# Optimization experiments

Measured on AMD Instinct MI355X. Metric: run time of the kernel, lower is better.

Reference implementation:

```python
import jax, jax.numpy as jnp
import numpy as np
import math

B, N, D, H, FF, L = 256, 200, 128, 8, 512, 2
KD = D // H  # key/val dim per head
NEG_INF = -1e30  # used via -jnp.inf where safe


def setup_inputs() -> dict:
    key = jax.random.key(0)
    ks = jax.random.split(key, 32)
    s = 0.08
    inp = {
        "coords": jax.random.uniform(ks[0], (B, N, 2), jnp.float32),
        "demand": jax.random.uniform(ks[1], (B, N), jnp.float32) * 0.01,
        # init embeddings
        "w_depot": jax.random.normal(ks[2], (2, D), jnp.float32) * s,
        "b_depot": jax.random.normal(ks[3], (D,), jnp.float32) * s,
        "w_init": jax.random.normal(ks[4], (3, D), jnp.float32) * s,
        "b_init": jax.random.normal(ks[5], (D,), jnp.float32) * s,
        # encoder layers (stacked over L)
        "Wq": jax.random.normal(ks[6], (L, H, D, KD), jnp.float32) * s,
        "Wk": jax.random.normal(ks[7], (L, H, D, KD), jnp.float32) * s,
        "Wv": jax.random.normal(ks[8], (L, H, D, KD), jnp.float32) * s,
        "Wo": jax.random.normal(ks[9], (L, H, KD, D), jnp.float32) * s,
        "ff1_w": jax.random.normal(ks[10], (L, D, FF), jnp.float32) * s,
        "ff1_b": jax.random.normal(ks[11], (L, FF), jnp.float32) * s,
        "ff2_w": jax.random.normal(ks[12], (L, FF, D), jnp.float32) * s,
        "ff2_b": jax.random.normal(ks[13], (L, D), jnp.float32) * s,
        "n1_g": jnp.ones((L, D), jnp.float32),
        "n1_b": jnp.zeros((L, D), jnp.float32),
        "n2_g": jnp.ones((L, D), jnp.float32),
        "n2_b": jnp.zeros((L, D), jnp.float32),
        # decoder projections
        "w_proj_nodes": jax.random.normal(ks[14], (D, 3 * D), jnp.float32) * s,
        "w_fixed": jax.random.normal(ks[15], (D, D), jnp.float32) * s,
        "w_step": jax.random.normal(ks[16], (D + 1, D), jnp.float32) * s,
        "w_out": jax.random.normal(ks[17], (D, D), jnp.float32) * s,
    }
    return inp


def _batch_norm(x, g, b):
    # torch BatchNorm1d on flattened (B*N, D), training-mode batch stats
    m = x.mean(axis=(0, 1))
    v = x.var(axis=(0, 1))
    return g * (x - m) * jax.lax.rsqrt(v + 1e-5) + b


def _mha(x, Wq, Wk, Wv, Wo):
    # x: [B,N,D]; W*: [H,D,KD]; Wo: [H,KD,D]
    Q = jnp.einsum('bni,hik->hbnk', x, Wq)
    K = jnp.einsum('bni,hik->hbnk', x, Wk)
    V = jnp.einsum('bni,hik->hbnk', x, Wv)
    scale = 1.0 / math.sqrt(KD)
    attn = jax.nn.softmax(scale * jnp.einsum('hbnk,hbmk->hbnm', Q, K), axis=-1)
    heads = jnp.einsum('hbnm,hbmk->hbnk', attn, V)
    return jnp.einsum('hbnk,hkd->bnd', heads, Wo)


def _forward(coords, demand, w_depot, b_depot, w_init, b_init,
             Wq, Wk, Wv, Wo, ff1_w, ff1_b, ff2_w, ff2_b,
             n1_g, n1_b, n2_g, n2_b, w_proj_nodes, w_fixed, w_step, w_out):
    # ---- _init_embed ----
    depot_emb = coords[:, :1, :2] @ w_depot + b_depot                      # [B,1,D]
    node_feat = jnp.concatenate([coords[:, 1:, :], demand[:, 1:, None]], -1)
    node_emb = node_feat @ w_init + b_init                                 # [B,N-1,D]
    h = jnp.concatenate([depot_emb, node_emb], axis=1)                     # [B,N,D]

    # ---- GraphAttentionEncoder ----
    for l in range(L):
        h = _batch_norm(h + _mha(h, Wq[l], Wk[l], Wv[l], Wo[l]), n1_g[l], n1_b[l])
        ff = jnp.maximum(h @ ff1_w[l] + ff1_b[l], 0.0) @ ff2_w[l] + ff2_b[l]
        h = _batch_norm(h + ff, n2_g[l], n2_b[l])

    # ---- _precompute ----
    fixed_ctx = h.mean(axis=1) @ w_fixed                                   # [B,D]
    proj = h @ w_proj_nodes                                                # [B,N,3D]
    gk, gv, lk = jnp.split(proj, 3, axis=-1)
    gk = gk.reshape(B, N, H, KD).transpose(2, 0, 1, 3)                     # [H,B,N,KD]
    gv = gv.reshape(B, N, H, KD).transpose(2, 0, 1, 3)                     # [H,B,N,KD]

    inv_sqrt_kd = 1.0 / math.sqrt(KD)
    inv_sqrt_d = 1.0 / math.sqrt(D)
    barange = jnp.arange(B)

    def step(carry, _):
        visited, cur, used = carry
        cur_emb = h[barange, cur]                                          # [B,D]
        ctx = jnp.concatenate([cur_emb, (1.0 - used)[:, None]], -1)        # [B,D+1]
        q = fixed_ctx + ctx @ w_step                                       # [B,D]
        qh = q.reshape(B, H, KD).transpose(1, 0, 2)                        # [H,B,KD]
        compat = jnp.einsum('hbk,hbnk->hbn', qh, gk) * inv_sqrt_kd         # [H,B,N]
        compat = jnp.where(visited[None], -jnp.inf, compat)                # mask_inner
        attn = jax.nn.softmax(compat, axis=-1)
        gl = jnp.einsum('hbn,hbnk->hbk', attn, gv)                         # [H,B,KD]
        final_q = gl.transpose(1, 0, 2).reshape(B, D) @ w_out              # [B,D]
        logits = jnp.einsum('bd,bnd->bn', final_q, lk) * inv_sqrt_d
        logits = jnp.tanh(logits) * 10.0                                   # tanh_clipping
        logits = jnp.where(visited, -jnp.inf, logits)                      # mask_logits
        logp = jax.nn.log_softmax(logits, axis=-1)                         # temp = 1.0
        sel = jnp.argmax(logp, axis=-1)                                    # greedy decode
        visited = visited.at[barange, sel].set(True)
        used = used + demand[barange, sel]
        return (visited, sel, used), (logp, sel)

    visited0 = jnp.zeros((B, N), bool).at[:, 0].set(True)  # start at depot
    cur0 = jnp.zeros((B,), jnp.int32)
    used0 = jnp.zeros((B,), jnp.float32)
    _, (logps, sels) = jax.lax.scan(step, (visited0, cur0, used0), None, length=N - 1)
    log_p = logps.transpose(1, 0, 2)   # [B, N-1, N]
    pi = sels.transpose(1, 0)          # [B, N-1]
    return log_p, pi


def reference(coords, demand, w_depot, b_depot, w_init, b_init,
              Wq, Wk, Wv, Wo, ff1_w, ff1_b, ff2_w, ff2_b,
              n1_g, n1_b, n2_g, n2_b, w_proj_nodes, w_fixed, w_step, w_out):
    return _forward(coords, demand, w_depot, b_depot, w_init, b_init,
                    Wq, Wk, Wv, Wo, ff1_w, ff1_b, ff2_w, ff2_b,
                    n1_g, n1_b, n2_g, n2_b, w_proj_nodes, w_fixed, w_step, w_out)
```

## Files before the change

kernel.cpp:

```cpp
#include <hip/hip_runtime.h>
#include <math.h>

#define NB 256
#define NN 200
#define ND 128
#define NH 8
#define NFF 512
#define MROWS (NB*NN)

#define NEG_BIG (-1.0e30f)

#define GBM 128
#define GBN 128
#define GBK 16
__global__ __launch_bounds__(256) void k_gemm(const float* __restrict__ A,
    const float* __restrict__ B, const float* __restrict__ bias,
    float* __restrict__ C, int M, int N, int K, int flags)
{
  __shared__ float As[GBK][GBM];
  __shared__ float Bs[GBK][GBN];
  const int t = threadIdx.x;
  const int tx = t & 15, ty = t >> 4;
  const int row0 = blockIdx.y * GBM, col0 = blockIdx.x * GBN;
  float acc[8][8] = {};
  for (int k0 = 0; k0 < K; k0 += GBK) {
    {
      int m = t >> 1, kb = (t & 1) * 8;
      const float* src = A + (size_t)(row0 + m) * K + k0 + kb;
      float4 v0 = *(const float4*)(src);
      float4 v1 = *(const float4*)(src + 4);
      As[kb+0][m] = v0.x; As[kb+1][m] = v0.y; As[kb+2][m] = v0.z; As[kb+3][m] = v0.w;
      As[kb+4][m] = v1.x; As[kb+5][m] = v1.y; As[kb+6][m] = v1.z; As[kb+7][m] = v1.w;
    }
    {
      int kk = t >> 4, nb = (t & 15) * 8;
      const float* src = B + (size_t)(k0 + kk) * N + col0 + nb;
      float4 v0 = *(const float4*)(src);
      float4 v1 = *(const float4*)(src + 4);
      *(float4*)&Bs[kk][nb]   = v0;
      *(float4*)&Bs[kk][nb+4] = v1;
    }
    __syncthreads();
    #pragma unroll
    for (int kk = 0; kk < GBK; ++kk) {
      float a[8], bv[8];
      *(float4*)&a[0]  = *(const float4*)&As[kk][ty*8];
      *(float4*)&a[4]  = *(const float4*)&As[kk][ty*8+4];
      *(float4*)&bv[0] = *(const float4*)&Bs[kk][tx*8];
      *(float4*)&bv[4] = *(const float4*)&Bs[kk][tx*8+4];
      #pragma unroll
      for (int i = 0; i < 8; ++i)
        #pragma unroll
        for (int j = 0; j < 8; ++j)
          acc[i][j] += a[i] * bv[j];
    }
    __syncthreads();
  }
  #pragma unroll
  for (int i = 0; i < 8; ++i) {
    int r = row0 + ty*8 + i;
    float* crow = C + (size_t)r * N + col0 + tx*8;
    #pragma unroll
    for (int j = 0; j < 8; ++j) {
      float v = acc[i][j];
      if (bias) v += bias[col0 + tx*8 + j];
      if (flags & 1) v += crow[j];
      if (flags & 2) v = fmaxf(v, 0.0f);
      crow[j] = v;
    }
  }
}

__global__ void k_pack_wqkv(const float* __restrict__ Wq, const float* __restrict__ Wk,
                            const float* __restrict__ Wv, float* __restrict__ outp)
{
  int idx = blockIdx.x * 256 + threadIdx.x;
  if (idx >= 2*128*384) return;
  int l = idx / (128*384); int r = idx % (128*384);
  int d = r / 384; int j = r % 384;
  int sel = j >> 7; int hk = j & 127; int h = hk >> 4; int k = hk & 15;
  const float* W = sel == 0 ? Wq : (sel == 1 ? Wk : Wv);
  outp[idx] = W[((size_t)(l*8 + h)*128 + d)*16 + k];
}

__global__ void k_init(const float* __restrict__ coords, const float* __restrict__ demand,
                       const float* __restrict__ w_depot, const float* __restrict__ b_depot,
                       const float* __restrict__ w_init, const float* __restrict__ b_init,
                       float* __restrict__ h)
{
  int idx = blockIdx.x * 256 + threadIdx.x;
  if (idx >= NB*NN*ND) return;
  int d = idx & 127; int bn = idx >> 7; int n = bn % NN; int b = bn / NN;
  float cx = coords[(size_t)(b*NN + n)*2], cy = coords[(size_t)(b*NN + n)*2 + 1];
  float v;
  if (n == 0) v = cx*w_depot[d] + cy*w_depot[128+d] + b_depot[d];
  else        v = cx*w_init[d] + cy*w_init[128+d] + demand[b*NN+n]*w_init[256+d] + b_init[d];
  h[idx] = v;
}

__global__ __launch_bounds__(256) void k_attn(const float* __restrict__ qkv, float* __restrict__ out)
{
  __shared__ float Qs[NN][16], Ks[NN][16], Vs[NN][16];
  __shared__ float Ss[32][NN];
  const int b = blockIdx.x >> 3, hd = blockIdx.x & 7;
  const int t = threadIdx.x;
  const float* base = qkv + (size_t)b * NN * 384 + hd * 16;
  for (int e = t; e < NN * 16; e += 256) {
    int n = e >> 4, k = e & 15;
    const float* p = base + (size_t)n * 384;
    Qs[n][k] = p[k];
    Ks[n][k] = p[128 + k];
    Vs[n][k] = p[256 + k];
  }
  __syncthreads();
  const int i = t >> 3;
  const int jl = t & 7;
  for (int i0 = 0; i0 < NN; i0 += 32) {
    int ii = i0 + i;
    if (ii < NN) {
      float4 q0 = *(const float4*)&Qs[ii][0];
      float4 q1 = *(const float4*)&Qs[ii][4];
      float4 q2 = *(const float4*)&Qs[ii][8];
      float4 q3 = *(const float4*)&Qs[ii][12];
      for (int j = jl; j < NN; j += 8) {
        const float* kr = &Ks[j][0];
        float s = q0.x*kr[0] + q0.y*kr[1] + q0.z*kr[2]  + q0.w*kr[3]
                + q1.x*kr[4] + q1.y*kr[5] + q1.z*kr[6]  + q1.w*kr[7]
                + q2.x*kr[8] + q2.y*kr[9] + q2.z*kr[10] + q2.w*kr[11]
                + q3.x*kr[12]+ q3.y*kr[13]+ q3.z*kr[14] + q3.w*kr[15];
        Ss[i][j] = s * 0.25f;
      }
      float m = -INFINITY;
      for (int j = jl; j < NN; j += 8) m = fmaxf(m, Ss[i][j]);
      m = fmaxf(m, __shfl_xor(m, 1));
      m = fmaxf(m, __shfl_xor(m, 2));
      m = fmaxf(m, __shfl_xor(m, 4));
      float sum = 0.f;
      for (int j = jl; j < NN; j += 8) { float p = expf(Ss[i][j] - m); Ss[i][j] = p; sum += p; }
      sum += __shfl_xor(sum, 1);
      sum += __shfl_xor(sum, 2);
      sum += __shfl_xor(sum, 4);
      float inv = 1.0f / sum;
      float a0 = 0.f, a1 = 0.f;
      int k0 = jl * 2;
      for (int j = 0; j < NN; ++j) {
        float p = Ss[i][j];
        a0 += p * Vs[j][k0];
        a1 += p * Vs[j][k0+1];
      }
      float* o = out + ((size_t)b * NN + ii) * ND + hd * 16 + k0;
      o[0] = a0 * inv; o[1] = a1 * inv;
    }
  }
}

__global__ __launch_bounds__(256) void k_bn_stats(const float* __restrict__ x, float* __restrict__ partial)
{
  int jb = blockIdx.x, t = threadIdx.x;
  int c = t & 127, half = t >> 7;
  const float* base = x + (size_t)jb * NN * ND;
  float s = 0.f, ss = 0.f;
  for (int r = half; r < NN; r += 2) {
    float v = base[(size_t)r * ND + c];
    s += v; ss += v * v;
  }
  __shared__ float s1[256], s2[256];
  s1[t] = s; s2[t] = ss;
  __syncthreads();
  if (t < 128) {
    partial[(size_t)jb*128 + t]         = s1[t] + s1[t+128];
    partial[32768 + (size_t)jb*128 + t] = s2[t] + s2[t+128];
  }
}

__global__ void k_bn_finish(const float* __restrict__ partial, const float* __restrict__ g,
                            const float* __restrict__ bb, float* __restrict__ scsh)
{
  int c = threadIdx.x;
  float s = 0.f, ss = 0.f;
  for (int jb = 0; jb < 256; ++jb) {
    s  += partial[jb*128 + c];
    ss += partial[32768 + jb*128 + c];
  }
  float mean = s * (1.0f/51200.0f);
  float var  = ss * (1.0f/51200.0f) - mean*mean;
  float sc = g[c] * rsqrtf(var + 1e-5f);
  scsh[c] = sc;
  scsh[128 + c] = bb[c] - mean * sc;
}

__global__ void k_bn_apply(float* __restrict__ x, const float* __restrict__ scsh)
{
  int idx = blockIdx.x * 256 + threadIdx.x;
  if (idx >= NB*NN*ND) return;
  int c = idx & 127;
  x[idx] = x[idx] * scsh[c] + scsh[128 + c];
}

__global__ __launch_bounds__(256) void k_mean(const float* __restrict__ h, float* __restrict__ meanh)
{
  int b = blockIdx.x, t = threadIdx.x;
  int d = t & 127, half = t >> 7;
  float s = 0.f;
  for (int n = half; n < NN; n += 2) s += h[((size_t)b*NN + n)*ND + d];
  __shared__ float sm[256];
  sm[t] = s;
  __syncthreads();
  if (t < 128) meanh[b*ND + t] = (sm[t] + sm[t+128]) * (1.0f/200.0f);
}

__global__ __launch_bounds__(512, 2) void k_decode(
    const float* __restrict__ proj, const float* __restrict__ hproj,
    const float* __restrict__ fixedc, const float* __restrict__ w_step,
    const float* __restrict__ w_out, const float* __restrict__ demand,
    float* __restrict__ out_logp, float* __restrict__ out_pi)
{
  const int b = blockIdx.x;
  const int t = threadIdx.x;
  __shared__ __align__(16) float q[ND];
  __shared__ __align__(16) float fq[ND];
  __shared__ float fc[ND], wlast[ND], dem[NN];
  __shared__ float cmat[NH][NN];
  __shared__ float logits[NN];
  __shared__ float glp[4][ND], gl[ND];
  __shared__ float fqp[4][ND];
  __shared__ int visited[NN];
  __shared__ int curs;
  __shared__ float useds;
  __shared__ float redf[8];
  __shared__ int redi[8];
  __shared__ float selv_s, lse_s;
  __shared__ int seln_s;

  const float* pb = proj + (size_t)b * NN * 384;
  const int g = t >> 4, j16 = t & 15;
  const int qi = j16 * 4;
  const int c = t >> 7, i = t & 127;

  if (t < ND) { fc[t] = fixedc[b*ND + t]; wlast[t] = w_step[128*ND + t]; }
  if (t < NN) { visited[t] = (t == 0) ? 1 : 0; dem[t] = demand[b*NN + t]; }
  if (t == 0) { curs = 0; useds = 0.0f; }

  float4 ka[7], kb_[7], la[7], lb[7];
  #pragma unroll
  for (int r = 0; r < 7; ++r) {
    int n = g + 32*r;
    if (n < NN) {
      const float* row = pb + (size_t)n * 384;
      ka[r]  = *(const float4*)(row + qi);
      kb_[r] = *(const float4*)(row + 64 + qi);
      la[r]  = *(const float4*)(row + 256 + qi);
      lb[r]  = *(const float4*)(row + 256 + 64 + qi);
    } else {
      ka[r] = float4{0,0,0,0}; kb_[r] = float4{0,0,0,0};
      la[r] = float4{0,0,0,0}; lb[r]  = float4{0,0,0,0};
    }
  }
  float gvr[50];
  #pragma unroll
  for (int k = 0; k < 50; ++k)
    gvr[k] = pb[(size_t)(c + 4*k)*384 + 128 + i];
  __syncthreads();

  for (int step = 0; step < NN - 1; ++step) {
    if (t < ND) q[t] = fc[t] + hproj[((size_t)b*NN + curs)*ND + t] + (1.0f - useds)*wlast[t];
    __syncthreads();

    {
      float4 qa = *(const float4*)(q + qi);
      float4 qb = *(const float4*)(q + 64 + qi);
      #pragma unroll
      for (int r = 0; r < 7; ++r) {
        int n = g + 32*r;
        if (n < NN) {
          float p0 = ka[r].x*qa.x + ka[r].y*qa.y + ka[r].z*qa.z + ka[r].w*qa.w;
          float p1 = kb_[r].x*qb.x + kb_[r].y*qb.y + kb_[r].z*qb.z + kb_[r].w*qb.w;
          p0 += __shfl_xor(p0, 1); p0 += __shfl_xor(p0, 2);
          p1 += __shfl_xor(p1, 1); p1 += __shfl_xor(p1, 2);
          if ((j16 & 3) == 0) {
            bool vis = visited[n] != 0;
            cmat[j16 >> 2][n]       = vis ? -1.0e30f : p0 * 0.25f;
            cmat[4 + (j16 >> 2)][n] = vis ? -1.0e30f : p1 * 0.25f;
          }
        }
      }
    }
    __syncthreads();

    if (t < 256) {
      int h = t >> 5, l5 = t & 31;
      float m = -INFINITY;
      for (int n = l5; n < NN; n += 32) m = fmaxf(m, cmat[h][n]);
      #pragma unroll
      for (int mm = 1; mm < 32; mm <<= 1) m = fmaxf(m, __shfl_xor(m, mm));
      float s = 0.f;
      for (int n = l5; n < NN; n += 32) { float p = expf(cmat[h][n] - m); cmat[h][n] = p; s += p; }
      #pragma unroll
      for (int mm = 1; mm < 32; mm <<= 1) s += __shfl_xor(s, mm);
      float inv = 1.0f / s;
      for (int n = l5; n < NN; n += 32) cmat[h][n] *= inv;
    }
    __syncthreads();

    {
      int hh = i >> 4;
      const float* pm = &cmat[hh][0];
      float acc = 0.f;
      #pragma unroll
      for (int k = 0; k < 50; ++k)
        acc += pm[c + 4*k] * gvr[k];
      glp[c][i] = acc;
    }
    __syncthreads();
    if (t < ND) gl[t] = (glp[0][t] + glp[1][t]) + (glp[2][t] + glp[3][t]);
    __syncthreads();

    {
      float acc = 0.f;
      const float* wb = w_out + (size_t)(c*32)*ND + i;
      #pragma unroll
      for (int k = 0; k < 32; ++k) acc += gl[c*32 + k] * wb[(size_t)k*ND];
      fqp[c][i] = acc;
    }
    __syncthreads();
    if (t < ND) fq[t] = (fqp[0][t] + fqp[1][t]) + (fqp[2][t] + fqp[3][t]);
    __syncthreads();

    {
      float4 fa = *(const float4*)(fq + qi);
      float4 fb = *(const float4*)(fq + 64 + qi);
      #pragma unroll
      for (int r = 0; r < 7; ++r) {
        int n = g + 32*r;
        if (n < NN) {
          float p = la[r].x*fa.x + la[r].y*fa.y + la[r].z*fa.z + la[r].w*fa.w
                  + lb[r].x*fb.x + lb[r].y*fb.y + lb[r].z*fb.z + lb[r].w*fb.w;
          p += __shfl_xor(p, 1); p += __shfl_xor(p, 2);
          p += __shfl_xor(p, 4); p += __shfl_xor(p, 8);
          if (j16 == 0)
            logits[n] = visited[n] ? -1.0e30f : tanhf(p * 0.088388347648318447f) * 10.0f;
        }
      }
    }
    __syncthreads();

    {
      float mv = (t < NN) ? logits[t] : -INFINITY;
      int   mn = (t < NN) ? t : 0x7fffffff;
      #pragma unroll
      for (int mm = 1; mm < 64; mm <<= 1) {
        float ov = __shfl_xor(mv, mm); int on = __shfl_xor(mn, mm);
        if (ov > mv || (ov == mv && on < mn)) { mv = ov; mn = on; }
      }
      if ((t & 63) == 0) { redf[t >> 6] = mv; redi[t >> 6] = mn; }
      __syncthreads();
      if (t == 0) {
        for (int w = 1; w < 8; ++w)
          if (redf[w] > mv || (redf[w] == mv && redi[w] < mn)) { mv = redf[w]; mn = redi[w]; }
        selv_s = mv; seln_s = mn;
      }
      __syncthreads();
    }
    {
      float gmax = selv_s;
      float se = (t < NN) ? expf(logits[t] - gmax) : 0.f;
      #pragma unroll
      for (int mm = 1; mm < 64; mm <<= 1) se += __shfl_xor(se, mm);
      if ((t & 63) == 0) redf[t >> 6] = se;
      __syncthreads();
      if (t == 0) {
        float s = 0.f;
        for (int w = 0; w < 8; ++w) s += redf[w];
        lse_s = gmax + logf(s);
      }
      __syncthreads();
    }
    float lse = lse_s;

    float* orow = out_logp + ((size_t)b*(NN-1) + step)*NN;
    if (t < NN) orow[t] = visited[t] ? NEG_BIG : logits[t] - lse;
    __syncthreads();
    if (t == 0) {
      int sel = seln_s;
      out_pi[(size_t)b*(NN-1) + step] = (float)sel;
      visited[sel] = 1;
      curs = sel;
      useds += dem[sel];
    }
    __syncthreads();
  }
}

extern "C" void kernel_launch(void* const* d_in, const int* in_sizes, int n_in,
                              void* d_out, int out_size, void* d_ws, size_t ws_size,
                              hipStream_t stream)
{
  (void)in_sizes; (void)n_in; (void)out_size; (void)ws_size;
  const float* coords  = (const float*)d_in[0];
  const float* demand  = (const float*)d_in[1];
  const float* w_depot = (const float*)d_in[2];
  const float* b_depot = (const float*)d_in[3];
  const float* w_init  = (const float*)d_in[4];
  const float* b_init  = (const float*)d_in[5];
  const float* Wq      = (const float*)d_in[6];
  const float* Wk      = (const float*)d_in[7];
  const float* Wv      = (const float*)d_in[8];
  const float* Wo      = (const float*)d_in[9];
  const float* ff1w    = (const float*)d_in[10];
  const float* ff1b    = (const float*)d_in[11];
  const float* ff2w    = (const float*)d_in[12];
  const float* ff2b    = (const float*)d_in[13];
  const float* n1g     = (const float*)d_in[14];
  const float* n1b     = (const float*)d_in[15];
  const float* n2g     = (const float*)d_in[16];
  const float* n2b     = (const float*)d_in[17];
  const float* wproj   = (const float*)d_in[18];
  const float* wfixed  = (const float*)d_in[19];
  const float* wstep   = (const float*)d_in[20];
  const float* wout    = (const float*)d_in[21];
  float* out = (float*)d_out;

  float* ws = (float*)d_ws;
  float* h       = ws;
  float* big     = h + 6553600;
  float* attnout = big + (size_t)MROWS * 384;
  float* hproj   = attnout;
  float* meanh   = big + 26214400;
  float* fixedc  = meanh + 32768;
  float* bnpart  = fixedc + 32768;
  float* scsh    = bnpart + 65536;
  float* wqkvp   = scsh + 256;

  k_pack_wqkv<<<(2*128*384 + 255)/256, 256, 0, stream>>>(Wq, Wk, Wv, wqkvp);
  k_init<<<(NB*NN*ND + 255)/256, 256, 0, stream>>>(coords, demand, w_depot, b_depot, w_init, b_init, h);

  for (int l = 0; l < 2; ++l) {
    k_gemm<<<dim3(384/GBN, MROWS/GBM), 256, 0, stream>>>(h, wqkvp + l*49152, nullptr, big, MROWS, 384, 128, 0);
    k_attn<<<NB*NH, 256, 0, stream>>>(big, attnout);
    k_gemm<<<dim3(1, MROWS/GBM), 256, 0, stream>>>(attnout, Wo + l*16384, nullptr, h, MROWS, 128, 128, 1);
    k_bn_stats<<<256, 256, 0, stream>>>(h, bnpart);
    k_bn_finish<<<1, 128, 0, stream>>>(bnpart, n1g + l*128, n1b + l*128, scsh);
    k_bn_apply<<<(NB*NN*ND + 255)/256, 256, 0, stream>>>(h, scsh);
    k_gemm<<<dim3(512/GBN, MROWS/GBM), 256, 0, stream>>>(h, ff1w + l*65536, ff1b + l*512, big, MROWS, 512, 128, 2);
    k_gemm<<<dim3(1, MROWS/GBM), 256, 0, stream>>>(big, ff2w + l*65536, ff2b + l*128, h, MROWS, 128, 512, 1);
    k_bn_stats<<<256, 256, 0, stream>>>(h, bnpart);
    k_bn_finish<<<1, 128, 0, stream>>>(bnpart, n2g + l*128, n2b + l*128, scsh);
    k_bn_apply<<<(NB*NN*ND + 255)/256, 256, 0, stream>>>(h, scsh);
  }

  k_mean<<<NB, 256, 0, stream>>>(h, meanh);
  k_gemm<<<dim3(1, 256/GBM), 256, 0, stream>>>(meanh, wfixed, nullptr, fixedc, 256, 128, 128, 0);
  k_gemm<<<dim3(384/GBN, MROWS/GBM), 256, 0, stream>>>(h, wproj, nullptr, big, MROWS, 384, 128, 0);
  k_gemm<<<dim3(1, MROWS/GBM), 256, 0, stream>>>(h, wstep, nullptr, hproj, MROWS, 128, 128, 0);

  k_decode<<<NB, 512, 0, stream>>>(big, hproj, fixedc, wstep, wout, demand,
                                   out, out + (size_t)NB*(NN-1)*NN);
}
```

Baseline: 3.461 ms.

## Cut decode-loop barriers with register query, online softmax-argmax, wider softmax

Restructures the per-step greedy decode loop. Each thread now builds the query in registers from preloaded fixed context and step weights, so the shared q buffer and its barrier go away. w_out is cached in registers, and the per-head softmax is spread over all 512 threads with register-held values. The argmax, max and sum-exp are merged into one online reduction, which removes several barriers per step. In exchange it uses more registers (launch bounds drop to 1 block per CU) and detects visited nodes by comparing logits to the sentinel value.

```diff
diff --git a/kernel.cpp b/kernel.cpp
--- a/kernel.cpp
+++ b/kernel.cpp
@@ -209,7 +209,7 @@
   if (t < 128) meanh[b*ND + t] = (sm[t] + sm[t+128]) * (1.0f/200.0f);
 }
 
-__global__ __launch_bounds__(512, 2) void k_decode(
+__global__ __launch_bounds__(512, 1) void k_decode(
     const float* __restrict__ proj, const float* __restrict__ hproj,
     const float* __restrict__ fixedc, const float* __restrict__ w_step,
     const float* __restrict__ w_out, const float* __restrict__ demand,
@@ -217,9 +217,8 @@
 {
   const int b = blockIdx.x;
   const int t = threadIdx.x;
-  __shared__ __align__(16) float q[ND];
   __shared__ __align__(16) float fq[ND];
-  __shared__ float fc[ND], wlast[ND], dem[NN];
+  __shared__ float dem[NN];
   __shared__ float cmat[NH][NN];
   __shared__ float logits[NN];
   __shared__ float glp[4][ND], gl[ND];
@@ -227,9 +226,9 @@
   __shared__ int visited[NN];
   __shared__ int curs;
   __shared__ float useds;
-  __shared__ float redf[8];
-  __shared__ int redi[8];
-  __shared__ float selv_s, lse_s;
+  __shared__ float redm[8], reds[8];
+  __shared__ int redn[8];
+  __shared__ float lse_s;
   __shared__ int seln_s;
 
   const float* pb = proj + (size_t)b * NN * 384;
@@ -237,7 +236,6 @@
   const int qi = j16 * 4;
   const int c = t >> 7, i = t & 127;
 
-  if (t < ND) { fc[t] = fixedc[b*ND + t]; wlast[t] = w_step[128*ND + t]; }
   if (t < NN) { visited[t] = (t == 0) ? 1 : 0; dem[t] = demand[b*NN + t]; }
   if (t == 0) { curs = 0; useds = 0.0f; }
 
@@ -260,15 +258,28 @@
   #pragma unroll
   for (int k = 0; k < 50; ++k)
     gvr[k] = pb[(size_t)(c + 4*k)*384 + 128 + i];
+  float wreg[32];
+  #pragma unroll
+  for (int k = 0; k < 32; ++k)
+    wreg[k] = w_out[(size_t)(c*32 + k)*ND + i];
+  float4 fcA = *(const float4*)(fixedc + (size_t)b*ND + qi);
+  float4 fcB = *(const float4*)(fixedc + (size_t)b*ND + 64 + qi);
+  float4 wlA = *(const float4*)(w_step + (size_t)128*ND + qi);
+  float4 wlB = *(const float4*)(w_step + (size_t)128*ND + 64 + qi);
+  const float* hpb = hproj + (size_t)b*NN*ND;
   __syncthreads();
 
   for (int step = 0; step < NN - 1; ++step) {
-    if (t < ND) q[t] = fc[t] + hproj[((size_t)b*NN + curs)*ND + t] + (1.0f - useds)*wlast[t];
-    __syncthreads();
-
-    {
-      float4 qa = *(const float4*)(q + qi);
-      float4 qb = *(const float4*)(q + 64 + qi);
+    {
+      int cur = curs; float ud = 1.0f - useds;
+      const float* hp = hpb + (size_t)cur*ND;
+      float4 ha = *(const float4*)(hp + qi);
+      float4 hb = *(const float4*)(hp + 64 + qi);
+      float4 qa, qb;
+      qa.x = fcA.x + ha.x + ud*wlA.x;  qa.y = fcA.y + ha.y + ud*wlA.y;
+      qa.z = fcA.z + ha.z + ud*wlA.z;  qa.w = fcA.w + ha.w + ud*wlA.w;
+      qb.x = fcB.x + hb.x + ud*wlB.x;  qb.y = fcB.y + hb.y + ud*wlB.y;
+      qb.z = fcB.z + hb.z + ud*wlB.z;  qb.w = fcB.w + hb.w + ud*wlB.w;
       #pragma unroll
       for (int r = 0; r < 7; ++r) {
         int n = g + 32*r;
@@ -287,18 +298,29 @@
     }
     __syncthreads();
 
-    if (t < 256) {
-      int h = t >> 5, l5 = t & 31;
-      float m = -INFINITY;
-      for (int n = l5; n < NN; n += 32) m = fmaxf(m, cmat[h][n]);
-      #pragma unroll
-      for (int mm = 1; mm < 32; mm <<= 1) m = fmaxf(m, __shfl_xor(m, mm));
-      float s = 0.f;
-      for (int n = l5; n < NN; n += 32) { float p = expf(cmat[h][n] - m); cmat[h][n] = p; s += p; }
-      #pragma unroll
-      for (int mm = 1; mm < 32; mm <<= 1) s += __shfl_xor(s, mm);
+    {
+      int w = t >> 6, l = t & 63;
+      float vv[4];
+      float m = -1.0e38f;
+      #pragma unroll
+      for (int j = 0; j < 4; ++j) {
+        int n = l + 64*j;
+        vv[j] = (n < NN) ? cmat[w][n] : -1.0e38f;
+        m = fmaxf(m, vv[j]);
+      }
+      #pragma unroll
+      for (int mm = 1; mm < 64; mm <<= 1) m = fmaxf(m, __shfl_xor(m, mm));
+      float ee[4]; float s = 0.f;
+      #pragma unroll
+      for (int j = 0; j < 4; ++j) { ee[j] = expf(vv[j] - m); s += ee[j]; }
+      #pragma unroll
+      for (int mm = 1; mm < 64; mm <<= 1) s += __shfl_xor(s, mm);
       float inv = 1.0f / s;
-      for (int n = l5; n < NN; n += 32) cmat[h][n] *= inv;
+      #pragma unroll
+      for (int j = 0; j < 4; ++j) {
+        int n = l + 64*j;
+        if (n < NN) cmat[w][n] = ee[j] * inv;
+      }
     }
     __syncthreads();
 
@@ -317,9 +339,8 @@
 
     {
       float acc = 0.f;
-      const float* wb = w_out + (size_t)(c*32)*ND + i;
-      #pragma unroll
-      for (int k = 0; k < 32; ++k) acc += gl[c*32 + k] * wb[(size_t)k*ND];
+      #pragma unroll
+      for (int k = 0; k < 32; ++k) acc += gl[c*32 + k] * wreg[k];
       fqp[c][i] = acc;
     }
     __syncthreads();
@@ -345,47 +366,58 @@
     __syncthreads();
 
     {
-      float mv = (t < NN) ? logits[t] : -INFINITY;
+      float mv = (t < NN) ? logits[t] : -1.0e38f;
       int   mn = (t < NN) ? t : 0x7fffffff;
+      float sv = (t < NN) ? 1.0f : 0.0f;
       #pragma unroll
       for (int mm = 1; mm < 64; mm <<= 1) {
-        float ov = __shfl_xor(mv, mm); int on = __shfl_xor(mn, mm);
-        if (ov > mv || (ov == mv && on < mn)) { mv = ov; mn = on; }
-      }
-      if ((t & 63) == 0) { redf[t >> 6] = mv; redi[t >> 6] = mn; }
-      __syncthreads();
+        float ov = __shfl_xor(mv, mm);
+        int   on = __shfl_xor(mn, mm);
+        float os = __shfl_xor(sv, mm);
+        bool take = (ov > mv) || (ov == mv && on < mn);
+        float mhi = take ? ov : mv;
+        float mlo = take ? mv : ov;
+        float shi = take ? os : sv;
+        float slo = take ? sv : os;
+        sv = shi + slo * expf(mlo - mhi);
+        mv = mhi;
+        mn = take ? on : mn;
+      }
+      if ((t & 63) == 0) { redm[t >> 6] = mv; redn[t >> 6] = mn; reds[t >> 6] = sv; }
+    }
+    __syncthreads();
+    if (t == 0) {
+      float mv = redm[0]; int mn = redn[0]; float sv = reds[0];
+      for (int w = 1; w < 8; ++w) {
+        float ov = redm[w]; int on = redn[w]; float os = reds[w];
+        bool take = (ov > mv) || (ov == mv && on < mn);
+        float mhi = take ? ov : mv;
+        float mlo = take ? mv : ov;
+        float shi = take ? os : sv;
+        float slo = take ? sv : os;
+        sv = shi + slo * expf(mlo - mhi);
+        mv = mhi;
+        mn = take ? on : mn;
+      }
+      seln_s = mn;
+      lse_s = mv + logf(sv);
+    }
+    __syncthreads();
+
+    {
+      float lse = lse_s;
+      float* orow = out_logp + ((size_t)b*(NN-1) + step)*NN;
+      if (t < NN) {
+        float lg = logits[t];
+        orow[t] = (lg == -1.0e30f) ? NEG_BIG : lg - lse;
+      }
       if (t == 0) {
-        for (int w = 1; w < 8; ++w)
-          if (redf[w] > mv || (redf[w] == mv && redi[w] < mn)) { mv = redf[w]; mn = redi[w]; }
-        selv_s = mv; seln_s = mn;
-      }
-      __syncthreads();
-    }
-    {
-      float gmax = selv_s;
-      float se = (t < NN) ? expf(logits[t] - gmax) : 0.f;
-      #pragma unroll
-      for (int mm = 1; mm < 64; mm <<= 1) se += __shfl_xor(se, mm);
-      if ((t & 63) == 0) redf[t >> 6] = se;
-      __syncthreads();
-      if (t == 0) {
-        float s = 0.f;
-        for (int w = 0; w < 8; ++w) s += redf[w];
-        lse_s = gmax + logf(s);
-      }
-      __syncthreads();
-    }
-    float lse = lse_s;
-
-    float* orow = out_logp + ((size_t)b*(NN-1) + step)*NN;
-    if (t < NN) orow[t] = visited[t] ? NEG_BIG : logits[t] - lse;
-    __syncthreads();
-    if (t == 0) {
-      int sel = seln_s;
-      out_pi[(size_t)b*(NN-1) + step] = (float)sel;
-      visited[sel] = 1;
-      curs = sel;
-      useds += dem[sel];
+        int sel = seln_s;
+        out_pi[(size_t)b*(NN-1) + step] = (float)sel;
+        visited[sel] = 1;
+        curs = sel;
+        useds += dem[sel];
+      }
     }
     __syncthreads();
   }
```

Measured after the change: 3.378 ms. -2.4%, faster.
